# Optimization experiments

Measured on AMD Instinct MI355X. Metric: run time of the kernel, lower is better.

## Reference

```python
import jax, jax.numpy as jnp
import numpy as np

NUM_MODES = 13   # 8192x8192 weight, mode_base=2, z-order-grouped pairs -> 13 modes of size 4
RANK = 8
MODE = 4
NUM_BASIS = 32
OUT_F = 8192
IN_F = 8192


def setup_inputs() -> dict:
    key = jax.random.key(0)
    k1, k2, k3 = jax.random.split(key, 3)
    basis_weights = jnp.clip(jax.random.normal(k1, (NUM_MODES, NUM_BASIS), jnp.float32), -3.0, 3.0)
    basis = jax.random.normal(k2, (NUM_BASIS, RANK, MODE, RANK), jnp.float32)
    rank_adapters = jax.random.uniform(k3, (NUM_MODES, RANK), jnp.float32, 0.5, 1.5)
    return {"basis_weights": basis_weights, "basis": basis, "rank_adapters": rank_adapters}


def _chain(cores):
    # cores: list of (r, m, r) tensors; returns chained (r, m^len, r)
    T = cores[0]
    for G in cores[1:]:
        T = jnp.einsum('aib,bjc->aijc', T, G).reshape(RANK, -1, RANK)
    return T


def reference(basis_weights, basis, rank_adapters):
    # decompress_cores: small GEMM over the shared basis, then rank-adapter scaling ('linear' act)
    cores = (basis_weights @ basis.reshape(NUM_BASIS, -1)).reshape(NUM_MODES, RANK, MODE, RANK)
    cores = cores * rank_adapters[:, :, None, None]
    core_list = [cores[m] for m in range(NUM_MODES)]
    # tensor-ring contraction with trace; split chain in half to bound intermediate memory
    half = NUM_MODES // 2
    L = _chain(core_list[:half])    # (r, MODE^6, r)
    R = _chain(core_list[half:])    # (r, MODE^7, r)
    w = jnp.einsum('aib,bja->ij', L, R).reshape((MODE,) * NUM_MODES)
    # inverse z-order reshape: each mode-4 dim = (row-bit, col-bit) interleaved pair
    w = w.reshape((2,) * (2 * NUM_MODES))
    perm = tuple(range(0, 2 * NUM_MODES, 2)) + tuple(range(1, 2 * NUM_MODES, 2))
    w = jnp.transpose(w, perm).reshape(OUT_F, IN_F)
    return w
```

## Files before the change

kernel.cpp:

```cpp
#include <hip/hip_runtime.h>


using bf16x8 = __attribute__((ext_vector_type(8))) short;
using u16x8  = __attribute__((ext_vector_type(8))) unsigned short;
using f32x16 = __attribute__((ext_vector_type(16))) float;

#define WS_LA    4096
#define WS_LB    20480
#define WS_RA    24576
#define WS_RB    40960
#define BOFF_AHI 262144
#define BOFF_ALO 786432
#define BOFF_BHI 1310720
#define BOFF_BLO 3407872

__device__ __forceinline__ unsigned short f2bf(float x) {
    unsigned int u = __builtin_bit_cast(unsigned int, x);
    u += 0x7fffu + ((u >> 16) & 1u);
    return (unsigned short)(u >> 16);
}
__device__ __forceinline__ float bf2f(unsigned short b) {
    unsigned int u = ((unsigned int)b) << 16;
    return __builtin_bit_cast(float, u);
}

__global__ void k_chains(const float* __restrict__ bw,
                         const float* __restrict__ basis,
                         const float* __restrict__ ra,
                         float* __restrict__ ws) {
    __shared__ float sCores[13 * 256];
    __shared__ float buf0[4096];
    __shared__ float buf1[4096];
    const int tid   = threadIdx.x;
    const int chain = blockIdx.x >> 4;
    const int slice = blockIdx.x & 15;

    const int s0   = (chain == 0) ? 0 : (chain == 1) ? 4 : (chain == 2) ? 6 : 10;
    const int nm   = (chain == 0) ? 4 : (chain == 1) ? 2 : (chain == 2) ? 4 : 3;
    const int wout = (chain == 0) ? WS_LA : (chain == 1) ? WS_LB
                   : (chain == 2) ? WS_RA : WS_RB;

    for (int e = tid; e < 13 * 256; e += 256) {
        int m    = e >> 8;
        int r1   = (e >> 5) & 7;
        int rest = e & 255;
        float s = 0.f;
#pragma unroll
        for (int n = 0; n < 32; ++n)
            s = fmaf(bw[m * 32 + n], basis[n * 256 + rest], s);
        sCores[e] = s * ra[m * 8 + r1];
    }
    __syncthreads();

    const float* src = &sCores[s0 * 256];
    int mcurlog = 2;
    float* dst = buf0;
    for (int step = 1; step < nm; ++step) {
        const float* core = &sCores[(s0 + step) * 256];
        const int moutlog = mcurlog + 2;
        const int mout    = 1 << moutlog;
        const int total   = 64 << moutlog;
        const bool last   = (step == nm - 1);
        const int sz   = total >> 4;
        const int ebeg = last ? slice * sz : 0;
        const int eend = last ? ebeg + sz  : total;
        for (int e = ebeg + tid; e < eend; e += 256) {
            int b  = e & 7;
            int im = (e >> 3) & (mout - 1);
            int a  = e >> (3 + moutlog);
            int i  = im >> 2, mm = im & 3;
            float s = 0.f;
#pragma unroll
            for (int c = 0; c < 8; ++c)
                s = fmaf(src[((a << mcurlog) + i) * 8 + c],
                         core[(c * 4 + mm) * 8 + b], s);
            if (last) ws[wout + e] = s;
            else      dst[e]       = s;
        }
        __syncthreads();
        src = dst;
        dst = (dst == buf0) ? buf1 : buf0;
        mcurlog = moutlog;
    }
}

__device__ __forceinline__ int ilv(int r, int c, int nb) {
    int v = 0;
    for (int t = 0; t < nb; ++t)
        v |= (((c >> t) & 1) << (2 * t)) | (((r >> t) & 1) << (2 * t + 1));
    return v;
}

__global__ void k_build(float* __restrict__ ws) {
    int idx = blockIdx.x * 256 + threadIdx.x;
    const float* LA = ws + WS_LA;
    const float* LB = ws + WS_LB;
    const float* RA = ws + WS_RA;
    const float* RB = ws + WS_RB;
    char* wsb = (char*)ws;
    unsigned short* Ahi = (unsigned short*)(wsb + BOFF_AHI);
    unsigned short* Alo = (unsigned short*)(wsb + BOFF_ALO);
    unsigned short* Bhi = (unsigned short*)(wsb + BOFF_BHI);
    unsigned short* Blo = (unsigned short*)(wsb + BOFF_BLO);

    float s[8];
    unsigned short* ph;
    unsigned short* pl;

    if (idx < 32768) {
        int a = idx & 7, m = idx >> 3;
        int ch = m & 63, rh = m >> 6;
        int i  = ilv(rh, ch, 6);
        int iA = i >> 4, iB = i & 15;
        const float* lap = LA + (a * 256 + iA) * 8;
        float la[8];
#pragma unroll
        for (int c = 0; c < 8; ++c) la[c] = lap[c];
#pragma unroll
        for (int b = 0; b < 8; ++b) s[b] = 0.f;
#pragma unroll
        for (int c = 0; c < 8; ++c) {
            const float* lbp = LB + (c * 16 + iB) * 8;
#pragma unroll
            for (int b = 0; b < 8; ++b)
                s[b] = fmaf(la[c], lbp[b], s[b]);
        }
        ph = Ahi + m * 64 + a * 8;
        pl = Alo + m * 64 + a * 8;
    } else {
        int t = idx - 32768;
        int a = t & 7, n = t >> 3;
        int rl = n >> 7, cl = n & 127;
        int j  = ilv(rl, cl, 7);
        int jA = j >> 6, jB = j & 63;
        float rb[8];
#pragma unroll
        for (int c = 0; c < 8; ++c) rb[c] = RB[(c * 64 + jB) * 8 + a];
#pragma unroll
        for (int b = 0; b < 8; ++b) {
            const float* rap = RA + (b * 256 + jA) * 8;
            float acc = 0.f;
#pragma unroll
            for (int c = 0; c < 8; ++c)
                acc = fmaf(rap[c], rb[c], acc);
            s[b] = acc;
        }
        ph = Bhi + n * 64 + a * 8;
        pl = Blo + n * 64 + a * 8;
    }

    u16x8 vh, vl;
#pragma unroll
    for (int b = 0; b < 8; ++b) {
        unsigned short h = f2bf(s[b]);
        vh[b] = h;
        vl[b] = f2bf(s[b] - bf2f(h));
    }
    *(u16x8*)ph = vh;
    *(u16x8*)pl = vl;
}

struct BF { bf16x8 h[4]; bf16x8 l[4]; };

__device__ __forceinline__ void load_half(const unsigned short* __restrict__ base,
                                          int nrow, int hi, bf16x8 (&d)[4]) {
    const unsigned short* p = base + (size_t)nrow * 64 + hi * 8;
#pragma unroll
    for (int kk = 0; kk < 4; ++kk)
        d[kk] = *(const bf16x8*)(p + kk * 16);
}

template<int I, bool LN>
__device__ __forceinline__ void tile_iter(
    const unsigned short* __restrict__ Bhi, const unsigned short* __restrict__ Blo,
    float* __restrict__ out,
    const bf16x8 (&A0h)[4], const bf16x8 (&A0l)[4],
    const bf16x8 (&A1h)[4], const bf16x8 (&A1l)[4],
    BF& cur, BF& nxt,
    int mb, int nbb, int w, int l31, int hi)
{
    const int nrown = nbb * 512 + (I + 1) * 128 + w * 32 + l31;
    if (LN) load_half(Bhi, nrown, hi, nxt.h);

    f32x16 acc0 = {0,0,0,0,0,0,0,0,0,0,0,0,0,0,0,0};
    f32x16 acc1 = {0,0,0,0,0,0,0,0,0,0,0,0,0,0,0,0};
#pragma unroll
    for (int kk = 0; kk < 4; ++kk) {
        acc0 = __builtin_amdgcn_mfma_f32_32x32x16_bf16(A0h[kk], cur.h[kk], acc0, 0, 0, 0);
        acc1 = __builtin_amdgcn_mfma_f32_32x32x16_bf16(A1h[kk], cur.h[kk], acc1, 0, 0, 0);
        acc0 = __builtin_amdgcn_mfma_f32_32x32x16_bf16(A0l[kk], cur.h[kk], acc0, 0, 0, 0);
        acc1 = __builtin_amdgcn_mfma_f32_32x32x16_bf16(A1l[kk], cur.h[kk], acc1, 0, 0, 0);
    }
    if (LN) load_half(Blo, nrown, hi, nxt.l);
#pragma unroll
    for (int kk = 0; kk < 4; ++kk) {
        acc0 = __builtin_amdgcn_mfma_f32_32x32x16_bf16(A0h[kk], cur.l[kk], acc0, 0, 0, 0);
        acc1 = __builtin_amdgcn_mfma_f32_32x32x16_bf16(A1h[kk], cur.l[kk], acc1, 0, 0, 0);
    }

    const int rl = nbb * 4 + I;
    float* obase  = out + (((size_t)(mb * 128 + rl)) << 13) + w * 32 + l31 + (size_t)hi * 512;
    float* obase2 = obase + 32 * 128;
#pragma unroll
    for (int r = 0; r < 16; ++r) {
        const int drow = (r & 3) + 8 * (r >> 2);
        __builtin_nontemporal_store(acc0[r], obase  + (size_t)drow * 128);
        __builtin_nontemporal_store(acc1[r], obase2 + (size_t)drow * 128);
    }
}

__global__ __launch_bounds__(256, 3) void k_out5(const float* __restrict__ ws,
                                                 float* __restrict__ out) {
    const char* wsb = (const char*)ws;
    const unsigned short* Ahi = (const unsigned short*)(wsb + BOFF_AHI);
    const unsigned short* Alo = (const unsigned short*)(wsb + BOFF_ALO);
    const unsigned short* Bhi = (const unsigned short*)(wsb + BOFF_BHI);
    const unsigned short* Blo = (const unsigned short*)(wsb + BOFF_BLO);

    const int tid  = threadIdx.x;
    const int lane = tid & 63;
    const int w    = tid >> 6;
    const int mb   = blockIdx.x >> 5;
    const int nbb  = blockIdx.x & 31;
    const int l31  = lane & 31;
    const int hi   = lane >> 5;

    bf16x8 A0h[4], A0l[4], A1h[4], A1l[4];
    {
        const int m0 = mb * 64 + l31;
        const int m1 = m0 + 32;
#pragma unroll
        for (int kk = 0; kk < 4; ++kk) {
            const int o = kk * 16 + hi * 8;
            A0h[kk] = *(const bf16x8*)(Ahi + m0 * 64 + o);
            A0l[kk] = *(const bf16x8*)(Alo + m0 * 64 + o);
            A1h[kk] = *(const bf16x8*)(Ahi + m1 * 64 + o);
            A1l[kk] = *(const bf16x8*)(Alo + m1 * 64 + o);
        }
    }

    BF b0, b1;
    {
        const int nrow0 = nbb * 512 + w * 32 + l31;
        load_half(Bhi, nrow0, hi, b0.h);
        load_half(Blo, nrow0, hi, b0.l);
    }

    tile_iter<0, true >(Bhi, Blo, out, A0h, A0l, A1h, A1l, b0, b1, mb, nbb, w, l31, hi);
    tile_iter<1, true >(Bhi, Blo, out, A0h, A0l, A1h, A1l, b1, b0, mb, nbb, w, l31, hi);
    tile_iter<2, true >(Bhi, Blo, out, A0h, A0l, A1h, A1l, b0, b1, mb, nbb, w, l31, hi);
    tile_iter<3, false>(Bhi, Blo, out, A0h, A0l, A1h, A1l, b1, b0, mb, nbb, w, l31, hi);
}

extern "C" void kernel_launch(void* const* d_in, const int* in_sizes, int n_in,
                              void* d_out, int out_size, void* d_ws, size_t ws_size,
                              hipStream_t stream) {
    const float* bw    = (const float*)d_in[0];
    const float* basis = (const float*)d_in[1];
    const float* ra    = (const float*)d_in[2];
    float* out = (float*)d_out;
    float* ws  = (float*)d_ws;

    k_chains<<<64,   256, 0, stream>>>(bw, basis, ra, ws);
    k_build <<<640,  256, 0, stream>>>(ws);
    k_out5  <<<2048, 256, 0, stream>>>(ws, out);
}
```

Measured before the change: 78.91 us.

## Remap waves to one M-tile each with eight N-subtiles for contiguous output rows

Each wave now owns a single 32-row M tile and walks eight 32-column N subtiles, where it previously held two M tiles across four N subtiles. The output store mapping changes so that each tile's writes land in contiguous 128-float segments within one output row group, aiming for better write coalescing of the 256MB fp32 output. The change roughly halves the A-fragment register footprint, which could help occupancy. In exchange, each B fragment is reused across only one M tile rather than two, so B loads per MFMA double.

```diff
diff --git a/kernel.cpp b/kernel.cpp
--- a/kernel.cpp
+++ b/kernel.cpp
@@ -174,42 +174,35 @@
 __device__ __forceinline__ void tile_iter(
     const unsigned short* __restrict__ Bhi, const unsigned short* __restrict__ Blo,
     float* __restrict__ out,
-    const bf16x8 (&A0h)[4], const bf16x8 (&A0l)[4],
-    const bf16x8 (&A1h)[4], const bf16x8 (&A1l)[4],
+    const bf16x8 (&Ah)[4], const bf16x8 (&Al)[4],
     BF& cur, BF& nxt,
-    int mb, int nbb, int w, int l31, int hi)
+    int nrowb, size_t rowb0, int mt, int hi)
 {
-    const int nrown = nbb * 512 + (I + 1) * 128 + w * 32 + l31;
+    const int nrown = nrowb + (I + 1) * 32;
     if (LN) load_half(Bhi, nrown, hi, nxt.h);
 
-    f32x16 acc0 = {0,0,0,0,0,0,0,0,0,0,0,0,0,0,0,0};
-    f32x16 acc1 = {0,0,0,0,0,0,0,0,0,0,0,0,0,0,0,0};
+    f32x16 acc = {0,0,0,0,0,0,0,0,0,0,0,0,0,0,0,0};
 #pragma unroll
     for (int kk = 0; kk < 4; ++kk) {
-        acc0 = __builtin_amdgcn_mfma_f32_32x32x16_bf16(A0h[kk], cur.h[kk], acc0, 0, 0, 0);
-        acc1 = __builtin_amdgcn_mfma_f32_32x32x16_bf16(A1h[kk], cur.h[kk], acc1, 0, 0, 0);
-        acc0 = __builtin_amdgcn_mfma_f32_32x32x16_bf16(A0l[kk], cur.h[kk], acc0, 0, 0, 0);
-        acc1 = __builtin_amdgcn_mfma_f32_32x32x16_bf16(A1l[kk], cur.h[kk], acc1, 0, 0, 0);
+        acc = __builtin_amdgcn_mfma_f32_32x32x16_bf16(Ah[kk], cur.h[kk], acc, 0, 0, 0);
+        acc = __builtin_amdgcn_mfma_f32_32x32x16_bf16(Al[kk], cur.h[kk], acc, 0, 0, 0);
     }
     if (LN) load_half(Blo, nrown, hi, nxt.l);
 #pragma unroll
     for (int kk = 0; kk < 4; ++kk) {
-        acc0 = __builtin_amdgcn_mfma_f32_32x32x16_bf16(A0h[kk], cur.l[kk], acc0, 0, 0, 0);
-        acc1 = __builtin_amdgcn_mfma_f32_32x32x16_bf16(A1h[kk], cur.l[kk], acc1, 0, 0, 0);
-    }
-
-    const int rl = nbb * 4 + I;
-    float* obase  = out + (((size_t)(mb * 128 + rl)) << 13) + w * 32 + l31 + (size_t)hi * 512;
-    float* obase2 = obase + 32 * 128;
+        acc = __builtin_amdgcn_mfma_f32_32x32x16_bf16(Ah[kk], cur.l[kk], acc, 0, 0, 0);
+    }
+
+    float* __restrict__ obase = out + ((rowb0 + (size_t)(I >> 2)) << 13)
+                              + (mt * 32 + 4 * hi) * 128 + (I & 3) * 32 + (nrowb & 31);
 #pragma unroll
     for (int r = 0; r < 16; ++r) {
         const int drow = (r & 3) + 8 * (r >> 2);
-        __builtin_nontemporal_store(acc0[r], obase  + (size_t)drow * 128);
-        __builtin_nontemporal_store(acc1[r], obase2 + (size_t)drow * 128);
-    }
-}
-
-__global__ __launch_bounds__(256, 3) void k_out5(const float* __restrict__ ws,
+        __builtin_nontemporal_store(acc[r], obase + (size_t)drow * 128);
+    }
+}
+
+__global__ __launch_bounds__(256, 3) void k_out9(const float* __restrict__ ws,
                                                  float* __restrict__ out) {
     const char* wsb = (const char*)ws;
     const unsigned short* Ahi = (const unsigned short*)(wsb + BOFF_AHI);
@@ -220,36 +213,39 @@
     const int tid  = threadIdx.x;
     const int lane = tid & 63;
     const int w    = tid >> 6;
+    const int mt   = w & 1;
+    const int nh   = w >> 1;
     const int mb   = blockIdx.x >> 5;
     const int nbb  = blockIdx.x & 31;
     const int l31  = lane & 31;
     const int hi   = lane >> 5;
 
-    bf16x8 A0h[4], A0l[4], A1h[4], A1l[4];
+    bf16x8 Ah[4], Al[4];
     {
-        const int m0 = mb * 64 + l31;
-        const int m1 = m0 + 32;
+        const int m0 = mb * 64 + mt * 32 + l31;
 #pragma unroll
         for (int kk = 0; kk < 4; ++kk) {
             const int o = kk * 16 + hi * 8;
-            A0h[kk] = *(const bf16x8*)(Ahi + m0 * 64 + o);
-            A0l[kk] = *(const bf16x8*)(Alo + m0 * 64 + o);
-            A1h[kk] = *(const bf16x8*)(Ahi + m1 * 64 + o);
-            A1l[kk] = *(const bf16x8*)(Alo + m1 * 64 + o);
-        }
-    }
+            Ah[kk] = *(const bf16x8*)(Ahi + m0 * 64 + o);
+            Al[kk] = *(const bf16x8*)(Alo + m0 * 64 + o);
+        }
+    }
+
+    const int nrowb = nbb * 512 + nh * 256 + l31;
+    const size_t rowb0 = (size_t)(mb * 128 + nbb * 4 + nh * 2);
 
     BF b0, b1;
-    {
-        const int nrow0 = nbb * 512 + w * 32 + l31;
-        load_half(Bhi, nrow0, hi, b0.h);
-        load_half(Blo, nrow0, hi, b0.l);
-    }
-
-    tile_iter<0, true >(Bhi, Blo, out, A0h, A0l, A1h, A1l, b0, b1, mb, nbb, w, l31, hi);
-    tile_iter<1, true >(Bhi, Blo, out, A0h, A0l, A1h, A1l, b1, b0, mb, nbb, w, l31, hi);
-    tile_iter<2, true >(Bhi, Blo, out, A0h, A0l, A1h, A1l, b0, b1, mb, nbb, w, l31, hi);
-    tile_iter<3, false>(Bhi, Blo, out, A0h, A0l, A1h, A1l, b1, b0, mb, nbb, w, l31, hi);
+    load_half(Bhi, nrowb, hi, b0.h);
+    load_half(Blo, nrowb, hi, b0.l);
+
+    tile_iter<0, true >(Bhi, Blo, out, Ah, Al, b0, b1, nrowb, rowb0, mt, hi);
+    tile_iter<1, true >(Bhi, Blo, out, Ah, Al, b1, b0, nrowb, rowb0, mt, hi);
+    tile_iter<2, true >(Bhi, Blo, out, Ah, Al, b0, b1, nrowb, rowb0, mt, hi);
+    tile_iter<3, true >(Bhi, Blo, out, Ah, Al, b1, b0, nrowb, rowb0, mt, hi);
+    tile_iter<4, true >(Bhi, Blo, out, Ah, Al, b0, b1, nrowb, rowb0, mt, hi);
+    tile_iter<5, true >(Bhi, Blo, out, Ah, Al, b1, b0, nrowb, rowb0, mt, hi);
+    tile_iter<6, true >(Bhi, Blo, out, Ah, Al, b0, b1, nrowb, rowb0, mt, hi);
+    tile_iter<7, false>(Bhi, Blo, out, Ah, Al, b1, b0, nrowb, rowb0, mt, hi);
 }
 
 extern "C" void kernel_launch(void* const* d_in, const int* in_sizes, int n_in,
@@ -263,5 +259,5 @@
 
     k_chains<<<64,   256, 0, stream>>>(bw, basis, ra, ws);
     k_build <<<640,  256, 0, stream>>>(ws);
-    k_out5  <<<2048, 256, 0, stream>>>(ws, out);
-}
+    k_out9  <<<2048, 256, 0, stream>>>(ws, out);
+}
```

After: 95.89 us. 1.22x slower.

## Stage output tiles in LDS and write contiguous 16-byte nontemporal stores

Applied to the files above, without the earlier changes.

The output kernel now stages each block's MFMA results in a 64KB shared-memory buffer and, after a barrier, writes two full contiguous output rows with 16-byte vector nontemporal stores. Previously each lane issued scalar strided stores. The grid doubles, with each block handling two tiles instead of four, and launch bounds drop to 2 blocks per CU. The goal is better write coalescing on a store-bound kernel, at the cost of LDS traffic, a sync, lower occupancy and possible LDS bank conflicts on the scatter.

```diff
diff --git a/kernel.cpp b/kernel.cpp
--- a/kernel.cpp
+++ b/kernel.cpp
@@ -3,6 +3,7 @@
 
 using bf16x8 = __attribute__((ext_vector_type(8))) short;
 using u16x8  = __attribute__((ext_vector_type(8))) unsigned short;
+using f32x4  = __attribute__((ext_vector_type(4))) float;
 using f32x16 = __attribute__((ext_vector_type(16))) float;
 
 #define WS_LA    4096
@@ -170,17 +171,16 @@
         d[kk] = *(const bf16x8*)(p + kk * 16);
 }
 
-template<int I, bool LN>
+template<bool LN>
 __device__ __forceinline__ void tile_iter(
     const unsigned short* __restrict__ Bhi, const unsigned short* __restrict__ Blo,
-    float* __restrict__ out,
+    float* __restrict__ sOut,
     const bf16x8 (&A0h)[4], const bf16x8 (&A0l)[4],
     const bf16x8 (&A1h)[4], const bf16x8 (&A1l)[4],
     BF& cur, BF& nxt,
-    int mb, int nbb, int w, int l31, int hi)
+    int nrow_next, int nt, int l31, int hi)
 {
-    const int nrown = nbb * 512 + (I + 1) * 128 + w * 32 + l31;
-    if (LN) load_half(Bhi, nrown, hi, nxt.h);
+    if (LN) load_half(Bhi, nrow_next, hi, nxt.h);
 
     f32x16 acc0 = {0,0,0,0,0,0,0,0,0,0,0,0,0,0,0,0};
     f32x16 acc1 = {0,0,0,0,0,0,0,0,0,0,0,0,0,0,0,0};
@@ -191,26 +191,27 @@
         acc0 = __builtin_amdgcn_mfma_f32_32x32x16_bf16(A0l[kk], cur.h[kk], acc0, 0, 0, 0);
         acc1 = __builtin_amdgcn_mfma_f32_32x32x16_bf16(A1l[kk], cur.h[kk], acc1, 0, 0, 0);
     }
-    if (LN) load_half(Blo, nrown, hi, nxt.l);
+    if (LN) load_half(Blo, nrow_next, hi, nxt.l);
 #pragma unroll
     for (int kk = 0; kk < 4; ++kk) {
         acc0 = __builtin_amdgcn_mfma_f32_32x32x16_bf16(A0h[kk], cur.l[kk], acc0, 0, 0, 0);
         acc1 = __builtin_amdgcn_mfma_f32_32x32x16_bf16(A1h[kk], cur.l[kk], acc1, 0, 0, 0);
     }
 
-    const int rl = nbb * 4 + I;
-    float* obase  = out + (((size_t)(mb * 128 + rl)) << 13) + w * 32 + l31 + (size_t)hi * 512;
-    float* obase2 = obase + 32 * 128;
+    const int base = (nt >> 2) * 8192 + (nt & 3) * 32 + l31;
 #pragma unroll
     for (int r = 0; r < 16; ++r) {
         const int drow = (r & 3) + 8 * (r >> 2);
-        __builtin_nontemporal_store(acc0[r], obase  + (size_t)drow * 128);
-        __builtin_nontemporal_store(acc1[r], obase2 + (size_t)drow * 128);
-    }
-}
-
-__global__ __launch_bounds__(256, 3) void k_out5(const float* __restrict__ ws,
-                                                 float* __restrict__ out) {
+        const int ch0  = drow + 4 * hi;
+        sOut[base + (ch0)      * 128] = acc0[r];
+        sOut[base + (ch0 + 32) * 128] = acc1[r];
+    }
+}
+
+__global__ __launch_bounds__(256, 2) void k_out10(const float* __restrict__ ws,
+                                                  float* __restrict__ out) {
+    __shared__ float sOut[16384];
+
     const char* wsb = (const char*)ws;
     const unsigned short* Ahi = (const unsigned short*)(wsb + BOFF_AHI);
     const unsigned short* Alo = (const unsigned short*)(wsb + BOFF_ALO);
@@ -220,8 +221,8 @@
     const int tid  = threadIdx.x;
     const int lane = tid & 63;
     const int w    = tid >> 6;
-    const int mb   = blockIdx.x >> 5;
-    const int nbb  = blockIdx.x & 31;
+    const int mb   = blockIdx.x >> 6;
+    const int nbb2 = blockIdx.x & 63;
     const int l31  = lane & 31;
     const int hi   = lane >> 5;
 
@@ -239,17 +240,25 @@
         }
     }
 
+    const int nr0 = nbb2 * 256 + w * 32 + l31;
     BF b0, b1;
-    {
-        const int nrow0 = nbb * 512 + w * 32 + l31;
-        load_half(Bhi, nrow0, hi, b0.h);
-        load_half(Blo, nrow0, hi, b0.l);
-    }
-
-    tile_iter<0, true >(Bhi, Blo, out, A0h, A0l, A1h, A1l, b0, b1, mb, nbb, w, l31, hi);
-    tile_iter<1, true >(Bhi, Blo, out, A0h, A0l, A1h, A1l, b1, b0, mb, nbb, w, l31, hi);
-    tile_iter<2, true >(Bhi, Blo, out, A0h, A0l, A1h, A1l, b0, b1, mb, nbb, w, l31, hi);
-    tile_iter<3, false>(Bhi, Blo, out, A0h, A0l, A1h, A1l, b1, b0, mb, nbb, w, l31, hi);
+    load_half(Bhi, nr0, hi, b0.h);
+    load_half(Blo, nr0, hi, b0.l);
+
+    tile_iter<true >(Bhi, Blo, sOut, A0h, A0l, A1h, A1l, b0, b1,
+                     nr0 + 128, w,     l31, hi);
+    tile_iter<false>(Bhi, Blo, sOut, A0h, A0l, A1h, A1l, b1, b0,
+                     0,         w + 4, l31, hi);
+
+    __syncthreads();
+
+    float* __restrict__ obase = out + (((size_t)(mb * 128 + nbb2 * 2)) << 13);
+#pragma unroll
+    for (int s = 0; s < 16; ++s) {
+        const int idx = w * 4096 + s * 256 + lane * 4;
+        const f32x4 v = *(const f32x4*)&sOut[idx];
+        __builtin_nontemporal_store(v, (f32x4*)(obase + idx));
+    }
 }
 
 extern "C" void kernel_launch(void* const* d_in, const int* in_sizes, int n_in,
@@ -263,5 +272,5 @@
 
     k_chains<<<64,   256, 0, stream>>>(bw, basis, ra, ws);
     k_build <<<640,  256, 0, stream>>>(ws);
-    k_out5  <<<2048, 256, 0, stream>>>(ws, out);
-}
+    k_out10 <<<4096, 256, 0, stream>>>(ws, out);
+}
```

Result: slower. 97.94 us (+24.1%).
